# Optimization experiments

Hardware: AMD Instinct MI355X
Metric: run time of the kernel (lower is better)

## Reference

```python
import jax, jax.numpy as jnp
import numpy as np

NUM_NODES = 8192
MUL = 64
ENV_P = 6
EPSILON = 1.0 / np.sqrt(17.0)  # 1/sqrt(1 + avg_num_neighbors), avg_num_neighbors=16


def _envelope(u, p=ENV_P):
    # polynomial smoothing envelope (cutoff at u = 1)
    a = -(p + 1) * (p + 2) / 2.0
    b = p * (p + 2)
    c = -p * (p + 1) / 2.0
    f = 1.0 + a * u ** p + b * u ** (p + 1) + c * u ** (p + 2)
    return jnp.where(u < 1.0, f, 0.0)


def setup_inputs() -> dict:
    key = jax.random.key(0)
    ks = jax.random.split(key, 9)
    E, F = 131072, 512
    vectors = jax.random.normal(ks[0], (E, 3), jnp.float32) * 0.35  # mostly inside cutoff
    x = jax.random.normal(ks[1], (E, F), jnp.float32)
    V = jax.random.normal(ks[2], (E, MUL, 4), jnp.float32)  # per mul-channel: [0e | 1o(3)]
    senders = jax.random.randint(ks[3], (E,), 0, NUM_NODES, jnp.int32)
    W_w = jax.random.normal(ks[4], (F, MUL), jnp.float32)
    W1 = jax.random.normal(ks[5], (F + 2 * MUL, 512), jnp.float32)
    W2 = jax.random.normal(ks[6], (512, 512), jnp.float32)
    W3 = jax.random.normal(ks[7], (512, 512), jnp.float32)
    W_lin = jax.random.normal(ks[8], (3 * MUL, MUL), jnp.float32)
    return {"vectors": vectors, "x": x, "V": V, "senders": senders,
            "W_w": W_w, "W1": W1, "W2": W2, "W3": W3, "W_lin": W_lin}


def reference(vectors, x, V, senders, W_w, W1, W2, W3, W_lin):
    E = vectors.shape[0]
    # edge-wise linear producing tensor-product weights  [E, MUL]
    w = (x @ W_w) / np.sqrt(x.shape[-1])
    # spherical harmonics (component norm), l = 0..1 of normalized vectors -> [E, 4]
    r = jnp.linalg.norm(vectors, axis=-1, keepdims=True)          # [E, 1]
    nhat = vectors / r
    Y = jnp.concatenate([jnp.ones((E, 1), vectors.dtype), np.sqrt(3.0) * nhat], axis=1)
    # weighted SH, scatter-sum over senders, gather back (map_back=True), scale by epsilon
    wY_e = w[:, :, None] * Y[:, None, :]                          # [E, MUL, 4]
    agg = jax.ops.segment_sum(wY_e, senders, num_segments=NUM_NODES)
    wY = agg[senders] * EPSILON                                   # [E, MUL, 4]
    # CG tensor product wY (0e+1o) x V (0e+1o), keep 0e and 1o outputs
    a0, a1 = wY[..., 0], wY[..., 1:]
    b0, b1 = V[..., 0], V[..., 1:]
    scal = jnp.concatenate(
        [a0 * b0, jnp.einsum('emi,emi->em', a1, b1) / np.sqrt(3.0)], axis=-1)  # [E, 2*MUL]
    vecs = jnp.concatenate(
        [a0[..., None] * b1, a1 * b0[..., None], jnp.cross(a1, b1) / np.sqrt(2.0)],
        axis=1)                                                   # [E, 3*MUL, 3]
    # concat scalar channel into invariants, 3-layer MLP (silu, linear last)
    xc = jnp.concatenate([x, scal], axis=1)                       # [E, 640]
    h = jax.nn.silu(xc @ W1 / np.sqrt(xc.shape[-1]))
    h = jax.nn.silu(h @ W2 / np.sqrt(h.shape[-1]))
    h = h @ W3 / np.sqrt(h.shape[-1])
    x_out = _envelope(r) * h                                      # [E, 512]
    # equivariant linear over the 1o multiplicity axis
    V_out = jnp.einsum('ekc,km->emc', vecs, W_lin) / np.sqrt(vecs.shape[1])  # [E, MUL, 3]
    return x_out, V_out
```

## Files before the change

kernel.cpp:

```cpp
#include <hip/hip_runtime.h>
#include <cstdint>
#include <cstddef>

#define E_TOT 131072
#define NNODES 8192

typedef __attribute__((ext_vector_type(8))) short bf16x8;
typedef __attribute__((ext_vector_type(4))) float f32x4;
typedef unsigned short u16;
typedef unsigned int u32;

__device__ __forceinline__ u16 f2bf(float f) {
    u32 u = __builtin_bit_cast(u32, f);
    u32 r = (u + 0x7FFFu + ((u >> 16) & 1u)) >> 16;
    return (u16)r;
}

__device__ __forceinline__ void gload16(const u16* g, u16* l) {
    __builtin_amdgcn_global_load_lds((const __attribute__((address_space(1))) void*)g,
                                     (__attribute__((address_space(3))) void*)l, 16, 0, 0);
}

__device__ __forceinline__ bf16x8 lds_frag(const u16* base, int row, int bytecol) {
    return *(const bf16x8*)((const char*)base + row * 128 + (bytecol ^ ((row & 7) << 4)));
}

__global__ void wconv_kernel(const float* __restrict__ src, u16* __restrict__ dst,
                             int K, int N) {
    int idx = blockIdx.x * 256 + threadIdx.x;
    if (idx >= N * K) return;
    int n = idx / K, k = idx - n * K;
    dst[idx] = f2bf(src[(size_t)k * N + n]);
}

__global__ void envy_kernel(const float* __restrict__ vectors, float* __restrict__ env,
                            float4* __restrict__ Y) {
    int e = blockIdx.x * 256 + threadIdx.x;
    float vx = vectors[3 * e + 0], vy = vectors[3 * e + 1], vz = vectors[3 * e + 2];
    float r2 = vx * vx + vy * vy + vz * vz;
    float r = sqrtf(r2);
    float u6 = r2 * r2 * r2;
    float f = 1.0f + u6 * (-28.0f + 48.0f * r - 21.0f * r2);
    env[e] = (r < 1.0f) ? f : 0.0f;
    float inv = 1.7320508075688772f / r;
    Y[e] = make_float4(1.0f, vx * inv, vy * inv, vz * inv);
}

__global__ void hist_kernel(const int* __restrict__ senders, int* __restrict__ cnt) {
    int e = blockIdx.x * 256 + threadIdx.x;
    atomicAdd(&cnt[senders[e]], 1);
}

__launch_bounds__(1024)
__global__ void scan_kernel(const int* __restrict__ cnt, int* __restrict__ off,
                            int* __restrict__ curs) {
    __shared__ int part[1024];
    const int t = threadIdx.x;
    int local[8];
    int s = 0;
#pragma unroll
    for (int j = 0; j < 8; ++j) { local[j] = cnt[t * 8 + j]; s += local[j]; }
    part[t] = s;
    __syncthreads();
    for (int d = 1; d < 1024; d <<= 1) {
        int v = (t >= d) ? part[t - d] : 0;
        __syncthreads();
        part[t] += v;
        __syncthreads();
    }
    int run = part[t] - s;
#pragma unroll
    for (int j = 0; j < 8; ++j) {
        off[t * 8 + j] = run;
        curs[t * 8 + j] = run;
        run += local[j];
    }
    if (t == 1023) off[8192] = run;
}

__global__ void permbuild_kernel(const int* __restrict__ senders, int* __restrict__ curs,
                                 int* __restrict__ perm) {
    int e = blockIdx.x * 256 + threadIdx.x;
    int s = senders[e];
    int p = atomicAdd(&curs[s], 1);
    perm[p] = e;
}

__launch_bounds__(256)
__global__ void gather_kernel(const float* __restrict__ w, const float4* __restrict__ Y,
                              const int* __restrict__ off, const int* __restrict__ perm,
                              float4* __restrict__ agg) {
    const int t = threadIdx.x;
    const int n = blockIdx.x * 4 + (t >> 6);
    const int m = t & 63;
    const int beg = off[n], end = off[n + 1];
    float4 acc = make_float4(0.f, 0.f, 0.f, 0.f);
    for (int i = beg; i < end; ++i) {
        int e = perm[i];
        float wv = w[(size_t)e * 64 + m];
        float4 y = Y[e];
        acc.x += wv * y.x; acc.y += wv * y.y; acc.z += wv * y.z; acc.w += wv * y.w;
    }
    agg[(size_t)n * 64 + m] = acc;
}

__launch_bounds__(256)
__global__ void wgemm_kernel(const float* __restrict__ x, const u16* __restrict__ Wt,
                             u16* __restrict__ XB, float* __restrict__ w) {
    __shared__ u16 As[128 * 72];
    __shared__ u16 Bs[64 * 72];
    const int e0 = blockIdx.x * 128;
    const int t = threadIdx.x, lane = t & 63, wid = t >> 6;
    const int lr = lane & 15, lh = lane >> 4;
    const int r8 = t >> 3, c8 = t & 7;
    f32x4 acc[2][4] = {};
    for (int kt = 0; kt < 8; ++kt) {
        const int kk = kt << 6;
#pragma unroll
        for (int i = 0; i < 4; ++i) {
            int row = i * 32 + r8;
            const float* gx = x + (size_t)(e0 + row) * 512 + kk + c8 * 8;
            float4 a = *(const float4*)gx;
            float4 b = *(const float4*)(gx + 4);
            union { u16 h[8]; uint4 v; } p;
            p.h[0] = f2bf(a.x); p.h[1] = f2bf(a.y); p.h[2] = f2bf(a.z); p.h[3] = f2bf(a.w);
            p.h[4] = f2bf(b.x); p.h[5] = f2bf(b.y); p.h[6] = f2bf(b.z); p.h[7] = f2bf(b.w);
            *(uint4*)((char*)As + row * 144 + c8 * 16) = p.v;
            *(uint4*)(XB + ((size_t)kt * E_TOT + e0 + row) * 64 + c8 * 8) = p.v;
        }
#pragma unroll
        for (int i = 0; i < 2; ++i) {
            int row = i * 32 + r8;
            const u16* g = Wt + (size_t)row * 512 + kk + c8 * 8;
            *(uint4*)((char*)Bs + row * 144 + c8 * 16) = *(const uint4*)g;
        }
        __syncthreads();
#pragma unroll
        for (int k2 = 0; k2 < 2; ++k2) {
            bf16x8 af[2], bfr[4];
#pragma unroll
            for (int m = 0; m < 2; ++m)
                af[m] = *(const bf16x8*)((const char*)As + (wid * 32 + m * 16 + lr) * 144 + k2 * 64 + lh * 16);
#pragma unroll
            for (int n = 0; n < 4; ++n)
                bfr[n] = *(const bf16x8*)((const char*)Bs + (n * 16 + lr) * 144 + k2 * 64 + lh * 16);
#pragma unroll
            for (int m = 0; m < 2; ++m)
#pragma unroll
                for (int n = 0; n < 4; ++n)
                    acc[m][n] = __builtin_amdgcn_mfma_f32_16x16x32_bf16(af[m], bfr[n], acc[m][n], 0, 0, 0);
        }
        __syncthreads();
    }
    const float s = 0.044194173824159216f;
#pragma unroll
    for (int m = 0; m < 2; ++m)
#pragma unroll
        for (int n = 0; n < 4; ++n)
#pragma unroll
            for (int j = 0; j < 4; ++j) {
                int e = e0 + wid * 32 + m * 16 + lh * 4 + j;
                w[(size_t)e * 64 + n * 16 + lr] = acc[m][n][j] * s;
            }
}

__launch_bounds__(256)
__global__ void edge_kernel(const int* __restrict__ senders, const float4* __restrict__ agg4,
                            const float4* __restrict__ V4, const u16* __restrict__ Wlt,
                            u16* __restrict__ scal, float* __restrict__ Vout) {
    __shared__ u16 a_lds[3][32][200];
    __shared__ u16 w_lds[64 * 200];
    const int t = threadIdx.x;
    const int e0 = blockIdx.x * 32;
#pragma unroll
    for (int i = 0; i < 6; ++i) {
        int c = i * 256 + t;
        int row = c / 24, off = (c % 24) * 8;
        *(uint4*)((char*)w_lds + row * 400 + off * 2) = ((const uint4*)Wlt)[c];
    }
    const float invs3 = 0.5773502691896258f;
    const float invs2 = 0.7071067811865476f;
    const float EPS = 0.24253562503633297f;
#pragma unroll
    for (int i = 0; i < 8; ++i) {
        int el = i * 4 + (t >> 6);
        int m = t & 63;
        int e = e0 + el;
        int s = senders[e];
        float4 a = agg4[(size_t)s * 64 + m];
        a.x *= EPS; a.y *= EPS; a.z *= EPS; a.w *= EPS;
        float4 b = V4[(size_t)e * 64 + m];
        float s0 = a.x * b.x;
        float s1 = (a.y * b.y + a.z * b.z + a.w * b.w) * invs3;
        scal[(size_t)e * 64 + m] = f2bf(s0);
        scal[(size_t)E_TOT * 64 + (size_t)e * 64 + m] = f2bf(s1);
        float cx = (a.z * b.w - a.w * b.z) * invs2;
        float cy = (a.w * b.y - a.y * b.w) * invs2;
        float cz = (a.y * b.z - a.z * b.y) * invs2;
        a_lds[0][el][m] = f2bf(a.x * b.y);
        a_lds[0][el][64 + m] = f2bf(a.y * b.x);
        a_lds[0][el][128 + m] = f2bf(cx);
        a_lds[1][el][m] = f2bf(a.x * b.z);
        a_lds[1][el][64 + m] = f2bf(a.z * b.x);
        a_lds[1][el][128 + m] = f2bf(cy);
        a_lds[2][el][m] = f2bf(a.x * b.w);
        a_lds[2][el][64 + m] = f2bf(a.w * b.x);
        a_lds[2][el][128 + m] = f2bf(cz);
    }
    __syncthreads();
    const int lane = t & 63, wid = t >> 6;
    const int lr = lane & 15, lh = lane >> 4;
    f32x4 acc[3][2] = {};
    for (int kt = 0; kt < 6; ++kt) {
        bf16x8 bfr = *(const bf16x8*)((const char*)w_lds + (wid * 16 + lr) * 400 + kt * 64 + lh * 16);
#pragma unroll
        for (int c = 0; c < 3; ++c)
#pragma unroll
            for (int m = 0; m < 2; ++m) {
                bf16x8 afr = *(const bf16x8*)((const char*)a_lds + ((c * 32 + m * 16 + lr) * 400) + kt * 64 + lh * 16);
                acc[c][m] = __builtin_amdgcn_mfma_f32_16x16x32_bf16(afr, bfr, acc[c][m], 0, 0, 0);
            }
    }
    __syncthreads();
    float* ot = (float*)a_lds;
    const float sc = 0.07216878364870323f;
#pragma unroll
    for (int c = 0; c < 3; ++c)
#pragma unroll
        for (int m = 0; m < 2; ++m)
#pragma unroll
            for (int j = 0; j < 4; ++j) {
                int row = m * 16 + lh * 4 + j;
                int mul = wid * 16 + lr;
                ot[row * 192 + mul * 3 + c] = acc[c][m][j] * sc;
            }
    __syncthreads();
    float4* vo = (float4*)(Vout + (size_t)e0 * 192);
#pragma unroll
    for (int i = 0; i < 6; ++i)
        vo[i * 256 + t] = ((float4*)ot)[i * 256 + t];
}

template <int MODE, int K>
__launch_bounds__(1024)
__global__ void mlp_gemm(const u16* __restrict__ A, const u16* __restrict__ A2,
                         const u16* __restrict__ Bt, const float scale,
                         const float* __restrict__ env,
                         u16* __restrict__ outb, float* __restrict__ outf) {
    constexpr int NKT = K >> 6;
    constexpr int NSTEP = NKT * 4;
    __shared__ u16 lds[2][2][256 * 64];
    const int b = blockIdx.x;
    const int t = threadIdx.x, lane = t & 63, wid = t >> 6;
    const int wm = wid >> 2, wn = wid & 3;
    const int lr = lane & 15, lh = lane >> 4;
    f32x4 acc[4][4] = {};

    auto issue = [&](int g) {
        const int tile = g / NKT;
        const int kt = g - tile * NKT;
        const int tid = b * 4 + tile;
        const int e0 = (tid >> 1) << 8;
        const int n0 = (tid & 1) << 8;
        const int kk = kt << 6;
        const int buf = g & 1;
        const u16* abase;
        size_t arow;
        if (A2 && kk >= 512) { abase = A2; arow = (size_t)((kk - 512) >> 6) * E_TOT + e0; }
        else                 { abase = A;  arow = (size_t)(kk >> 6) * E_TOT + e0; }
#pragma unroll
        for (int i = 0; i < 2; ++i) {
            const int c = i * 1024 + t;
            const int rowin = c >> 3;
            const int scol = ((c & 7) ^ (rowin & 7)) << 3;
            gload16(abase + (arow + rowin) * 64 + scol,
                    (u16*)&lds[buf][0][0] + (size_t)c * 8);
        }
#pragma unroll
        for (int i = 0; i < 2; ++i) {
            const int c = i * 1024 + t;
            const int rowin = c >> 3;
            const int scol = ((c & 7) ^ (rowin & 7)) << 3;
            gload16(Bt + (size_t)(n0 + rowin) * K + kk + scol,
                    (u16*)&lds[buf][1][0] + (size_t)c * 8);
        }
    };

    issue(0);
    issue(1);
    for (int g = 0; g < NSTEP; ++g) {
        const int tile = g / NKT;
        const int kt = g - tile * NKT;
        if (g + 1 >= NSTEP)           asm volatile("s_waitcnt vmcnt(0)\ns_barrier" ::: "memory");
        else if (kt <= 1 && tile > 0) asm volatile("s_waitcnt vmcnt(8)\ns_barrier" ::: "memory");
        else                          asm volatile("s_waitcnt vmcnt(4)\ns_barrier" ::: "memory");
        const u16* Ab = lds[g & 1][0];
        const u16* Bb = lds[g & 1][1];
        __builtin_amdgcn_s_setprio(1);
#pragma unroll
        for (int k2 = 0; k2 < 2; ++k2) {
            bf16x8 af[4], bfr[4];
#pragma unroll
            for (int m = 0; m < 4; ++m)
                af[m] = lds_frag(Ab, wm * 64 + m * 16 + lr, k2 * 64 + lh * 16);
#pragma unroll
            for (int n = 0; n < 4; ++n)
                bfr[n] = lds_frag(Bb, wn * 64 + n * 16 + lr, k2 * 64 + lh * 16);
#pragma unroll
            for (int m = 0; m < 4; ++m)
#pragma unroll
                for (int n = 0; n < 4; ++n)
                    acc[m][n] = __builtin_amdgcn_mfma_f32_16x16x32_bf16(af[m], bfr[n], acc[m][n], 0, 0, 0);
        }
        __builtin_amdgcn_s_setprio(0);
        asm volatile("s_waitcnt lgkmcnt(0)\ns_barrier" ::: "memory");
        if (g + 2 < NSTEP) issue(g + 2);
        if (kt == NKT - 1) {
            const int tid = b * 4 + tile;
            const int e0 = (tid >> 1) << 8;
            const int n0 = (tid & 1) << 8;
#pragma unroll
            for (int m = 0; m < 4; ++m) {
#pragma unroll
                for (int j = 0; j < 4; ++j) {
                    const int row = e0 + wm * 64 + m * 16 + lh * 4 + j;
                    float ev = (MODE == 1) ? env[row] : 0.0f;
#pragma unroll
                    for (int n = 0; n < 4; ++n) {
                        const int col = n0 + wn * 64 + n * 16 + lr;
                        float v = acc[m][n][j] * scale;
                        if (MODE == 0) {
                            float sv = v / (1.0f + __expf(-v));
                            outb[((size_t)(col >> 6) * E_TOT + row) * 64 + (col & 63)] = f2bf(sv);
                        } else {
                            outf[(size_t)row * 512 + col] = v * ev;
                        }
                    }
                }
            }
#pragma unroll
            for (int m = 0; m < 4; ++m)
#pragma unroll
                for (int n = 0; n < 4; ++n)
                    acc[m][n] = f32x4{0.f, 0.f, 0.f, 0.f};
        }
    }
}

extern "C" void kernel_launch(void* const* d_in, const int* in_sizes, int n_in,
                              void* d_out, int out_size, void* d_ws, size_t ws_size,
                              hipStream_t stream) {
    const float* vectors = (const float*)d_in[0];
    const float* x       = (const float*)d_in[1];
    const float* V       = (const float*)d_in[2];
    const int*   senders = (const int*)d_in[3];
    const float* W_w     = (const float*)d_in[4];
    const float* W1      = (const float*)d_in[5];
    const float* W2      = (const float*)d_in[6];
    const float* W3      = (const float*)d_in[7];
    const float* W_lin   = (const float*)d_in[8];
    float* out = (float*)d_out;
    char* ws = (char*)d_ws;

    u16*    XB   = (u16*)(ws + 0x0);
    u16*    H1   = (u16*)(ws + 0x8000000);
    u16*    SCAL = (u16*)(ws + 0x10000000);
    float*  AGG  = (float*)(ws + 0x12000000);
    float*  ENV  = (float*)(ws + 0x12800000);
    float4* Yb   = (float4*)(ws + 0x12880000);
    float*  Wbuf = (float*)(ws + 0x12A80000);
    u16*    WT   = (u16*)(ws + 0x14A80000);
    u16* Wwt = WT;
    u16* W1t = Wwt + 64 * 512;
    u16* W2t = W1t + 512 * 640;
    u16* W3t = W2t + 512 * 512;
    u16* Wlt = W3t + 512 * 512;
    u16* H2 = XB;
    int* COUNT = (int*)(ws + 0x15000000);
    int* OFF   = (int*)(ws + 0x15010000);
    int* CURS  = (int*)(ws + 0x15020000);
    int* PERM  = (int*)(ws + 0x15030000);

    hipMemsetAsync(COUNT, 0, NNODES * sizeof(int), stream);

    wconv_kernel<<<(64 * 512) / 256, 256, 0, stream>>>(W_w, Wwt, 512, 64);
    wconv_kernel<<<(512 * 640) / 256, 256, 0, stream>>>(W1, W1t, 640, 512);
    wconv_kernel<<<(512 * 512) / 256, 256, 0, stream>>>(W2, W2t, 512, 512);
    wconv_kernel<<<(512 * 512) / 256, 256, 0, stream>>>(W3, W3t, 512, 512);
    wconv_kernel<<<(64 * 192) / 256, 256, 0, stream>>>(W_lin, Wlt, 192, 64);

    envy_kernel<<<E_TOT / 256, 256, 0, stream>>>(vectors, ENV, Yb);

    hist_kernel<<<E_TOT / 256, 256, 0, stream>>>(senders, COUNT);
    scan_kernel<<<1, 1024, 0, stream>>>(COUNT, OFF, CURS);
    permbuild_kernel<<<E_TOT / 256, 256, 0, stream>>>(senders, CURS, PERM);

    wgemm_kernel<<<E_TOT / 128, 256, 0, stream>>>(x, Wwt, XB, Wbuf);
    gather_kernel<<<NNODES / 4, 256, 0, stream>>>(Wbuf, Yb, OFF, PERM, (float4*)AGG);

    edge_kernel<<<E_TOT / 32, 256, 0, stream>>>(senders, (const float4*)AGG, (const float4*)V,
                                                Wlt, SCAL, out + (size_t)E_TOT * 512);

    const float s640 = 0.03952847075210474f;
    const float s512 = 0.044194173824159216f;
    mlp_gemm<0, 640><<<256, 1024, 0, stream>>>(XB, SCAL, W1t, s640, nullptr, H1, nullptr);
    mlp_gemm<0, 512><<<256, 1024, 0, stream>>>(H1, nullptr, W2t, s512, nullptr, H2, nullptr);
    mlp_gemm<1, 512><<<256, 1024, 0, stream>>>(H2, nullptr, W3t, s512, ENV, nullptr, out);
}
```

Before: 572.4 us.

## Switch MLP GEMM to K=32 steps with triple-buffered LDS and one barrier

The MLP GEMM main loop now advances 32 K-elements per step instead of 64 and uses a three-slot LDS ring instead of double buffering. This lets the next tile's global-to-LDS load be issued right after fragments are read, and drops the second barrier per iteration. A new swizzled fragment layout packs two rows per 128-byte LDS line. The cost is twice as many loop iterations and barriers over K, plus hand-tuned vmcnt counts that must match the outstanding-load pattern exactly, including the epilogue stores at tile boundaries.

```diff
diff --git a/kernel.cpp b/kernel.cpp
--- a/kernel.cpp
+++ b/kernel.cpp
@@ -23,6 +23,12 @@
 
 __device__ __forceinline__ bf16x8 lds_frag(const u16* base, int row, int bytecol) {
     return *(const bf16x8*)((const char*)base + row * 128 + (bytecol ^ ((row & 7) << 4)));
+}
+
+__device__ __forceinline__ bf16x8 lds_frag32(const u16* base, int row, int lh) {
+    const int ldsrow = row >> 1;
+    const int gr = (((row & 1) << 2) + lh) ^ (ldsrow & 7);
+    return *(const bf16x8*)((const char*)base + ldsrow * 128 + gr * 16);
 }
 
 __global__ void wconv_kernel(const float* __restrict__ src, u16* __restrict__ dst,
@@ -247,75 +253,66 @@
                          const u16* __restrict__ Bt, const float scale,
                          const float* __restrict__ env,
                          u16* __restrict__ outb, float* __restrict__ outf) {
-    constexpr int NKT = K >> 6;
+    constexpr int NKT = K >> 5;
     constexpr int NSTEP = NKT * 4;
-    __shared__ u16 lds[2][2][256 * 64];
+    __shared__ u16 lds[3 * 16384];
     const int b = blockIdx.x;
     const int t = threadIdx.x, lane = t & 63, wid = t >> 6;
     const int wm = wid >> 2, wn = wid & 3;
     const int lr = lane & 15, lh = lane >> 4;
     f32x4 acc[4][4] = {};
 
+    const int ldsrow = t >> 3;
+    const int sg = t & 7;
+    const int og = sg ^ (ldsrow & 7);
+    const int half = og >> 2;
+    const int k8 = og & 3;
+    const int arow = ldsrow * 2 + half;
+
     auto issue = [&](int g) {
         const int tile = g / NKT;
-        const int kt = g - tile * NKT;
+        const int kt32 = g - tile * NKT;
         const int tid = b * 4 + tile;
         const int e0 = (tid >> 1) << 8;
         const int n0 = (tid & 1) << 8;
-        const int kk = kt << 6;
-        const int buf = g & 1;
+        const int kk = kt32 << 5;
+        u16* slot = lds + (g % 3) * 16384;
         const u16* abase;
-        size_t arow;
-        if (A2 && kk >= 512) { abase = A2; arow = (size_t)((kk - 512) >> 6) * E_TOT + e0; }
-        else                 { abase = A;  arow = (size_t)(kk >> 6) * E_TOT + e0; }
-#pragma unroll
-        for (int i = 0; i < 2; ++i) {
-            const int c = i * 1024 + t;
-            const int rowin = c >> 3;
-            const int scol = ((c & 7) ^ (rowin & 7)) << 3;
-            gload16(abase + (arow + rowin) * 64 + scol,
-                    (u16*)&lds[buf][0][0] + (size_t)c * 8);
-        }
-#pragma unroll
-        for (int i = 0; i < 2; ++i) {
-            const int c = i * 1024 + t;
-            const int rowin = c >> 3;
-            const int scol = ((c & 7) ^ (rowin & 7)) << 3;
-            gload16(Bt + (size_t)(n0 + rowin) * K + kk + scol,
-                    (u16*)&lds[buf][1][0] + (size_t)c * 8);
-        }
+        int kt64;
+        if (A2 && kk >= 512) { abase = A2; kt64 = (kt32 - 16) >> 1; }
+        else                 { abase = A;  kt64 = kt32 >> 1; }
+        const int khalf = kt32 & 1;
+        gload16(abase + ((size_t)kt64 * E_TOT + e0 + arow) * 64 + khalf * 32 + k8 * 8,
+                slot + (size_t)t * 8);
+        gload16(Bt + (size_t)(n0 + arow) * K + kk + k8 * 8,
+                slot + 8192 + (size_t)t * 8);
     };
 
     issue(0);
     issue(1);
     for (int g = 0; g < NSTEP; ++g) {
         const int tile = g / NKT;
-        const int kt = g - tile * NKT;
-        if (g + 1 >= NSTEP)           asm volatile("s_waitcnt vmcnt(0)\ns_barrier" ::: "memory");
-        else if (kt <= 1 && tile > 0) asm volatile("s_waitcnt vmcnt(8)\ns_barrier" ::: "memory");
-        else                          asm volatile("s_waitcnt vmcnt(4)\ns_barrier" ::: "memory");
-        const u16* Ab = lds[g & 1][0];
-        const u16* Bb = lds[g & 1][1];
+        const int kt32 = g - tile * NKT;
+        if (g + 1 >= NSTEP)             asm volatile("s_waitcnt vmcnt(0)\ns_barrier" ::: "memory");
+        else if (kt32 <= 1 && tile > 0) asm volatile("s_waitcnt vmcnt(34)\ns_barrier" ::: "memory");
+        else                            asm volatile("s_waitcnt vmcnt(2)\ns_barrier" ::: "memory");
+        const u16* slot = lds + (g % 3) * 16384;
+        bf16x8 af[4], bfr[4];
+#pragma unroll
+        for (int m = 0; m < 4; ++m)
+            af[m] = lds_frag32(slot, wm * 64 + m * 16 + lr, lh);
+#pragma unroll
+        for (int n = 0; n < 4; ++n)
+            bfr[n] = lds_frag32(slot + 8192, wn * 64 + n * 16 + lr, lh);
+        if (g + 2 < NSTEP) issue(g + 2);
         __builtin_amdgcn_s_setprio(1);
 #pragma unroll
-        for (int k2 = 0; k2 < 2; ++k2) {
-            bf16x8 af[4], bfr[4];
-#pragma unroll
-            for (int m = 0; m < 4; ++m)
-                af[m] = lds_frag(Ab, wm * 64 + m * 16 + lr, k2 * 64 + lh * 16);
+        for (int m = 0; m < 4; ++m)
 #pragma unroll
             for (int n = 0; n < 4; ++n)
-                bfr[n] = lds_frag(Bb, wn * 64 + n * 16 + lr, k2 * 64 + lh * 16);
-#pragma unroll
-            for (int m = 0; m < 4; ++m)
-#pragma unroll
-                for (int n = 0; n < 4; ++n)
-                    acc[m][n] = __builtin_amdgcn_mfma_f32_16x16x32_bf16(af[m], bfr[n], acc[m][n], 0, 0, 0);
-        }
+                acc[m][n] = __builtin_amdgcn_mfma_f32_16x16x32_bf16(af[m], bfr[n], acc[m][n], 0, 0, 0);
         __builtin_amdgcn_s_setprio(0);
-        asm volatile("s_waitcnt lgkmcnt(0)\ns_barrier" ::: "memory");
-        if (g + 2 < NSTEP) issue(g + 2);
-        if (kt == NKT - 1) {
+        if (kt32 == NKT - 1) {
             const int tid = b * 4 + tile;
             const int e0 = (tid >> 1) << 8;
             const int n0 = (tid & 1) << 8;
```

After: 585.3 us. 1.02x slower.

## Retile MLP GEMM to 128x512 blocks with 512 threads and wider per-wave N

Applied to the files above, without the earlier changes.

Changes the MLP GEMM block tile from 256x256 (16 waves) to 128 rows by the full 512 columns (8 waves, each computing 64x128). Activations are now fetched once per row tile instead of once per column half, cutting global A traffic. The full B slice is loaded per k-step, which raises B traffic and LDS use to about 160 KB. Fewer waves per CU and double the accumulators per thread risk lower latency hiding and register pressure.

```diff
diff --git a/kernel.cpp b/kernel.cpp
--- a/kernel.cpp
+++ b/kernel.cpp
@@ -242,47 +242,46 @@
 }
 
 template <int MODE, int K>
-__launch_bounds__(1024)
+__launch_bounds__(512)
 __global__ void mlp_gemm(const u16* __restrict__ A, const u16* __restrict__ A2,
                          const u16* __restrict__ Bt, const float scale,
                          const float* __restrict__ env,
                          u16* __restrict__ outb, float* __restrict__ outf) {
     constexpr int NKT = K >> 6;
     constexpr int NSTEP = NKT * 4;
-    __shared__ u16 lds[2][2][256 * 64];
+    __shared__ u16 lds[81920];
     const int b = blockIdx.x;
     const int t = threadIdx.x, lane = t & 63, wid = t >> 6;
     const int wm = wid >> 2, wn = wid & 3;
     const int lr = lane & 15, lh = lane >> 4;
-    f32x4 acc[4][4] = {};
+    f32x4 acc[4][8] = {};
 
     auto issue = [&](int g) {
         const int tile = g / NKT;
         const int kt = g - tile * NKT;
-        const int tid = b * 4 + tile;
-        const int e0 = (tid >> 1) << 8;
-        const int n0 = (tid & 1) << 8;
+        const int mt = b * 4 + tile;
+        const int e0 = mt << 7;
         const int kk = kt << 6;
-        const int buf = g & 1;
+        u16* buf = lds + (g & 1) * 40960;
         const u16* abase;
-        size_t arow;
-        if (A2 && kk >= 512) { abase = A2; arow = (size_t)((kk - 512) >> 6) * E_TOT + e0; }
-        else                 { abase = A;  arow = (size_t)(kk >> 6) * E_TOT + e0; }
+        int kt64;
+        if (A2 && kk >= 512) { abase = A2; kt64 = (kk - 512) >> 6; }
+        else                 { abase = A;  kt64 = kk >> 6; }
 #pragma unroll
         for (int i = 0; i < 2; ++i) {
-            const int c = i * 1024 + t;
+            const int c = i * 512 + t;
             const int rowin = c >> 3;
             const int scol = ((c & 7) ^ (rowin & 7)) << 3;
-            gload16(abase + (arow + rowin) * 64 + scol,
-                    (u16*)&lds[buf][0][0] + (size_t)c * 8);
-        }
-#pragma unroll
-        for (int i = 0; i < 2; ++i) {
-            const int c = i * 1024 + t;
+            gload16(abase + ((size_t)kt64 * E_TOT + e0 + rowin) * 64 + scol,
+                    buf + (size_t)c * 8);
+        }
+#pragma unroll
+        for (int i = 0; i < 8; ++i) {
+            const int c = i * 512 + t;
             const int rowin = c >> 3;
             const int scol = ((c & 7) ^ (rowin & 7)) << 3;
-            gload16(Bt + (size_t)(n0 + rowin) * K + kk + scol,
-                    (u16*)&lds[buf][1][0] + (size_t)c * 8);
+            gload16(Bt + (size_t)rowin * K + kk + scol,
+                    buf + 8192 + (size_t)c * 8);
         }
     };
 
@@ -291,34 +290,32 @@
     for (int g = 0; g < NSTEP; ++g) {
         const int tile = g / NKT;
         const int kt = g - tile * NKT;
-        if (g + 1 >= NSTEP)           asm volatile("s_waitcnt vmcnt(0)\ns_barrier" ::: "memory");
-        else if (kt <= 1 && tile > 0) asm volatile("s_waitcnt vmcnt(8)\ns_barrier" ::: "memory");
-        else                          asm volatile("s_waitcnt vmcnt(4)\ns_barrier" ::: "memory");
-        const u16* Ab = lds[g & 1][0];
-        const u16* Bb = lds[g & 1][1];
+        if (g + 1 >= NSTEP) asm volatile("s_waitcnt vmcnt(0)\ns_barrier" ::: "memory");
+        else                asm volatile("s_waitcnt vmcnt(10)\ns_barrier" ::: "memory");
+        const u16* Ab = lds + (g & 1) * 40960;
+        const u16* Bb = Ab + 8192;
         __builtin_amdgcn_s_setprio(1);
 #pragma unroll
         for (int k2 = 0; k2 < 2; ++k2) {
-            bf16x8 af[4], bfr[4];
+            bf16x8 af[4], bfr[8];
 #pragma unroll
             for (int m = 0; m < 4; ++m)
                 af[m] = lds_frag(Ab, wm * 64 + m * 16 + lr, k2 * 64 + lh * 16);
 #pragma unroll
-            for (int n = 0; n < 4; ++n)
-                bfr[n] = lds_frag(Bb, wn * 64 + n * 16 + lr, k2 * 64 + lh * 16);
+            for (int n = 0; n < 8; ++n)
+                bfr[n] = lds_frag(Bb, wn * 128 + n * 16 + lr, k2 * 64 + lh * 16);
 #pragma unroll
             for (int m = 0; m < 4; ++m)
 #pragma unroll
-                for (int n = 0; n < 4; ++n)
+                for (int n = 0; n < 8; ++n)
                     acc[m][n] = __builtin_amdgcn_mfma_f32_16x16x32_bf16(af[m], bfr[n], acc[m][n], 0, 0, 0);
         }
         __builtin_amdgcn_s_setprio(0);
         asm volatile("s_waitcnt lgkmcnt(0)\ns_barrier" ::: "memory");
         if (g + 2 < NSTEP) issue(g + 2);
         if (kt == NKT - 1) {
-            const int tid = b * 4 + tile;
-            const int e0 = (tid >> 1) << 8;
-            const int n0 = (tid & 1) << 8;
+            const int mt = b * 4 + tile;
+            const int e0 = mt << 7;
 #pragma unroll
             for (int m = 0; m < 4; ++m) {
 #pragma unroll
@@ -326,8 +323,8 @@
                     const int row = e0 + wm * 64 + m * 16 + lh * 4 + j;
                     float ev = (MODE == 1) ? env[row] : 0.0f;
 #pragma unroll
-                    for (int n = 0; n < 4; ++n) {
-                        const int col = n0 + wn * 64 + n * 16 + lr;
+                    for (int n = 0; n < 8; ++n) {
+                        const int col = wn * 128 + n * 16 + lr;
                         float v = acc[m][n][j] * scale;
                         if (MODE == 0) {
                             float sv = v / (1.0f + __expf(-v));
@@ -341,7 +338,7 @@
 #pragma unroll
             for (int m = 0; m < 4; ++m)
 #pragma unroll
-                for (int n = 0; n < 4; ++n)
+                for (int n = 0; n < 8; ++n)
                     acc[m][n] = f32x4{0.f, 0.f, 0.f, 0.f};
         }
     }
@@ -403,7 +400,7 @@
 
     const float s640 = 0.03952847075210474f;
     const float s512 = 0.044194173824159216f;
-    mlp_gemm<0, 640><<<256, 1024, 0, stream>>>(XB, SCAL, W1t, s640, nullptr, H1, nullptr);
-    mlp_gemm<0, 512><<<256, 1024, 0, stream>>>(H1, nullptr, W2t, s512, nullptr, H2, nullptr);
-    mlp_gemm<1, 512><<<256, 1024, 0, stream>>>(H2, nullptr, W3t, s512, ENV, nullptr, out);
-}
+    mlp_gemm<0, 640><<<256, 512, 0, stream>>>(XB, SCAL, W1t, s640, nullptr, H1, nullptr);
+    mlp_gemm<0, 512><<<256, 512, 0, stream>>>(H1, nullptr, W2t, s512, nullptr, H2, nullptr);
+    mlp_gemm<1, 512><<<256, 512, 0, stream>>>(H2, nullptr, W3t, s512, ENV, nullptr, out);
+}
```

New measurement: 596.7 us. 1.04x slower.
